# Kernel tuning notes

Hardware: AMD Instinct MI355X
Metric: run time of the kernel (lower is better)

## Reference

```python
import jax, jax.numpy as jnp
import numpy as np

N = 8192       # batch_size
D = 128        # embedding dim
C = 1000       # num classes
EPS = 1e-8     # torch CosineSimilarity eps


def setup_inputs() -> dict:
    key = jax.random.key(0)
    k1, k2, k3, k4 = jax.random.split(key, 4)
    inst_embed = jax.random.normal(k1, (N, D), dtype=jnp.float32)
    proxy = jax.random.normal(k2, (N, D), dtype=jnp.float32)
    # binary mask marking same-class (non-negative) pairs, stored as float
    negative_mask = (jax.random.uniform(k3, (N, C)) < 0.5).astype(jnp.float32)
    labels = jax.random.randint(k4, (N,), 0, C)
    temperature = jnp.float32(0.07)
    margin = jnp.float32(0.0)
    return {
        'inst_embed': inst_embed,
        'proxy': proxy,
        'negative_mask': negative_mask,
        'labels': labels,
        'temperature': temperature,
        'margin': margin,
    }


def _remove_diag(M):
    # M: [h, h] -> [h, h-1], dropping the diagonal, row-major order (as torch bool-mask view)
    h = M.shape[0]
    j = jnp.arange(h - 1)[None, :]
    i = jnp.arange(h)[:, None]
    cols = j + (j >= i)  # skip column i in row i
    return jnp.take_along_axis(M, cols, axis=1)


def _l2_normalize(x):
    return x / jnp.maximum(jnp.linalg.norm(x, axis=-1, keepdims=True), EPS)


def reference(inst_embed, proxy, negative_mask, labels, temperature, margin):
    negative_mask = negative_mask.T                       # [C, N]
    xn = _l2_normalize(inst_embed)                        # [N, D]
    sim = xn @ xn.T                                       # [N, N] cosine similarity matrix
    instance_zone = jnp.exp((_remove_diag(sim) - margin) / temperature)  # [N, N-1]
    pn = _l2_normalize(proxy)
    inst2proxy_positive = jnp.exp((jnp.sum(xn * pn, axis=-1) - margin) / temperature)  # [N]
    # pos_collected_numerator == True branch
    mask_4_remove_negatives = _remove_diag(negative_mask[labels])        # [N, N-1]
    inst2inst_positives = instance_zone * mask_4_remove_negatives
    numerator = inst2proxy_positive + inst2inst_positives.sum(axis=1)
    denominator = inst2proxy_positive + instance_zone.sum(axis=1)
    criterion = -jnp.log(temperature * (numerator / denominator)).mean()
    return criterion
```

## Files before the change

kernel.cpp:

```cpp
#include <hip/hip_runtime.h>
#include <hip/hip_bf16.h>

typedef unsigned short u16;
typedef unsigned int   u32;
typedef unsigned long long u64;
typedef __attribute__((ext_vector_type(8))) short short8;
typedef __attribute__((ext_vector_type(4))) float float4v;

#define N 8192
#define D 128
#define C 1000
#define TILE 128
#define LDT 136
#define NW64 (N / 64)
#define JQ 4
#define JW (JQ * 2)

__global__ void norm_kernel(const float* __restrict__ x, const float* __restrict__ pr,
                            u16* __restrict__ xnb, float* __restrict__ p_out,
                            float* __restrict__ den, float* __restrict__ num,
                            const float* __restrict__ tp, const float* __restrict__ mp) {
    const int wave = threadIdx.x >> 6;
    const int lane = threadIdx.x & 63;
    const int row  = blockIdx.x * 4 + wave;

    const float2* xr  = (const float2*)(x  + (size_t)row * D);
    const float2* prr = (const float2*)(pr + (size_t)row * D);
    float2 xv = xr[lane];
    float2 pv = prr[lane];

    float sx  = xv.x * xv.x + xv.y * xv.y;
    float sp  = pv.x * pv.x + pv.y * pv.y;
    float sxp = xv.x * pv.x + xv.y * pv.y;
    #pragma unroll
    for (int off = 32; off; off >>= 1) {
        sx  += __shfl_xor(sx,  off);
        sp  += __shfl_xor(sp,  off);
        sxp += __shfl_xor(sxp, off);
    }
    float nx = fmaxf(sqrtf(sx), 1e-8f);
    float np = fmaxf(sqrtf(sp), 1e-8f);
    float inv = 1.0f / nx;

    __hip_bfloat16 b0 = __float2bfloat16(xv.x * inv);
    __hip_bfloat16 b1 = __float2bfloat16(xv.y * inv);
    ((__hip_bfloat162*)xnb)[(size_t)row * 64 + lane] = __halves2bfloat162(b0, b1);

    if (lane == 0) {
        float T = tp[0], M = mp[0];
        p_out[row] = __expf((sxp / (nx * np) - M) / T);
        den[row] = 0.0f;
        num[row] = 0.0f;
    }
}

__global__ void pack_kernel(const float* __restrict__ nm, u64* __restrict__ packed) {
    __shared__ u32 Ls[64 * 65];
    const int lane = threadIdx.x & 63;
    const int wv   = threadIdx.x >> 6;
    const int jt   = blockIdx.x;
    const int lt   = blockIdx.y;
    const int j0   = jt * 64;
    const int l    = lt * 64 + lane;
    const bool lv  = l < C;

    #pragma unroll
    for (int rr = 0; rr < 16; rr++) {
        const int r = wv * 16 + rr;
        float v = lv ? nm[(size_t)(j0 + r) * C + l] : 0.0f;
        Ls[r * 65 + lane] = (v > 0.5f) ? 1u : 0u;
    }
    __syncthreads();
    #pragma unroll
    for (int cc = 0; cc < 16; cc++) {
        const int c = wv * 16 + cc;
        u64 m = __ballot(Ls[lane * 65 + c] != 0u);
        if (lane == 0 && (lt * 64 + c) < C)
            packed[(size_t)(lt * 64 + c) * NW64 + jt] = m;
    }
}

template <bool DIAG>
__device__ __forceinline__ void epilogue(const float4v acc[4][4], const u64* __restrict__ Ms,
                                         float dacc[4][4], float nacc[4][4],
                                         int wr, int wc, int kq, int m0,
                                         int ibase, int jbase, int q,
                                         float kA, float kB) {
    #pragma unroll
    for (int tm = 0; tm < 4; tm++) {
        #pragma unroll
        for (int r = 0; r < 4; r++) {
            const int lrow = wr * 64 + tm * 16 + kq * 4 + r;
            const u64 ws = Ms[lrow * JW + q * 2 + wc] >> m0;
            const u32 wlo = (u32)ws, whi = (u32)(ws >> 32);
            const int gi = ibase + lrow;
            #pragma unroll
            for (int tn = 0; tn < 4; tn++) {
                float e = __expf(fmaf(acc[tm][tn][r], kA, kB));
                if (DIAG) {
                    const int gj = jbase + wc * 64 + tn * 16 + m0;
                    if (gi == gj) e = 0.0f;
                }
                dacc[tm][r] += e;
                const u32 bit = ((tn < 2) ? (wlo >> (tn * 16)) : (whi >> ((tn - 2) * 16))) & 1u;
                nacc[tm][r] = fmaf((float)bit, e, nacc[tm][r]);
            }
        }
    }
}

__global__ __launch_bounds__(256, 2)
void cc_main(const u16* __restrict__ xnb, const int* __restrict__ labels,
             const u64* __restrict__ packed,
             float* __restrict__ den, float* __restrict__ num,
             const float* __restrict__ tp, const float* __restrict__ mp) {
    __shared__ u16 As[TILE * LDT];
    __shared__ u64 Ms[TILE * JW];

    const int tid  = threadIdx.x;
    const int lane = tid & 63;
    const int wv   = tid >> 6;
    const int wr   = wv >> 1;
    const int wc   = wv & 1;
    const int m0   = lane & 15;
    const int kq   = lane >> 4;
    const int ibase  = blockIdx.x * TILE;
    const int jsplit = blockIdx.y;

    const float T = tp[0];
    const float M = mp[0];
    const float kA = 1.0f / T;
    const float kB = -M / T;

    {
        const int r = tid >> 1, h = tid & 1;
        const uint4* src = (const uint4*)(xnb + (size_t)(ibase + r) * D + h * 64);
        uint4* dst = (uint4*)(As + r * LDT + h * 64);
        #pragma unroll
        for (int qq = 0; qq < 8; qq++) dst[qq] = src[qq];
    }
    #pragma unroll
    for (int t = 0; t < 4; t++) {
        const int idx = t * 256 + tid;
        const int row = idx >> 3, h = idx & 7;
        const int lab = labels[ibase + row];
        Ms[idx] = packed[(size_t)lab * NW64 + jsplit * JW + h];
    }
    __syncthreads();

    float dacc[4][4] = {};
    float nacc[4][4] = {};

    const u16* Abase = As + (wr * 64 + m0) * LDT + kq * 8;

    for (int q = 0; q < JQ; q++) {
        const int jt = jsplit * JQ + q;
        const int jbase = jt * TILE;

        const u16* Bp = xnb + (size_t)(jbase + wc * 64 + m0) * D + kq * 8;

        float4v acc[4][4];
        #pragma unroll
        for (int a = 0; a < 4; a++)
            #pragma unroll
            for (int b = 0; b < 4; b++)
                acc[a][b] = (float4v){0.f, 0.f, 0.f, 0.f};

        #pragma unroll
        for (int kk = 0; kk < 4; kk++) {
            short8 b_f[4];
            #pragma unroll
            for (int tn = 0; tn < 4; tn++)
                b_f[tn] = *(const short8*)(Bp + tn * (16 * D) + kk * 32);
            short8 a_f[4];
            #pragma unroll
            for (int tm = 0; tm < 4; tm++)
                a_f[tm] = *(const short8*)(Abase + tm * (16 * LDT) + kk * 32);
            #pragma unroll
            for (int tm = 0; tm < 4; tm++)
                #pragma unroll
                for (int tn = 0; tn < 4; tn++)
                    acc[tm][tn] = __builtin_amdgcn_mfma_f32_16x16x32_bf16(
                        a_f[tm], b_f[tn], acc[tm][tn], 0, 0, 0);
        }

        if (jt == blockIdx.x)
            epilogue<true >(acc, Ms, dacc, nacc, wr, wc, kq, m0, ibase, jbase, q, kA, kB);
        else
            epilogue<false>(acc, Ms, dacc, nacc, wr, wc, kq, m0, ibase, jbase, q, kA, kB);
    }

    #pragma unroll
    for (int tm = 0; tm < 4; tm++) {
        #pragma unroll
        for (int r = 0; r < 4; r++) {
            float d = dacc[tm][r], n = nacc[tm][r];
            #pragma unroll
            for (int off = 1; off < 16; off <<= 1) {
                d += __shfl_xor(d, off);
                n += __shfl_xor(n, off);
            }
            if (m0 == 0) {
                const int gi = ibase + wr * 64 + tm * 16 + kq * 4 + r;
                atomicAdd(&den[gi], d);
                atomicAdd(&num[gi], n);
            }
        }
    }
}

__global__ void loss_kernel(const float* __restrict__ p, const float* __restrict__ den,
                            const float* __restrict__ num, float* __restrict__ out,
                            const float* __restrict__ tp) {
    __shared__ float red[16];
    const float T = tp[0];
    float s = 0.0f;
    #pragma unroll
    for (int t = 0; t < N / 1024; t++) {
        const int i = t * 1024 + threadIdx.x;
        float pi = p[i];
        s += -__logf(T * (pi + num[i]) / (pi + den[i]));
    }
    #pragma unroll
    for (int off = 32; off; off >>= 1) s += __shfl_xor(s, off);
    const int lane = threadIdx.x & 63, wv = threadIdx.x >> 6;
    if (lane == 0) red[wv] = s;
    __syncthreads();
    if (wv == 0) {
        float t = (lane < 16) ? red[lane] : 0.0f;
        #pragma unroll
        for (int off = 8; off; off >>= 1) t += __shfl_xor(t, off);
        if (lane == 0) out[0] = t / (float)N;
    }
}

extern "C" void kernel_launch(void* const* d_in, const int* in_sizes, int n_in,
                              void* d_out, int out_size, void* d_ws, size_t ws_size,
                              hipStream_t stream) {
    (void)in_sizes; (void)n_in; (void)out_size; (void)ws_size;
    const float* inst   = (const float*)d_in[0];
    const float* proxy  = (const float*)d_in[1];
    const float* nm     = (const float*)d_in[2];
    const int*   labels = (const int*)d_in[3];
    const float* temp   = (const float*)d_in[4];
    const float* marg   = (const float*)d_in[5];
    float* out = (float*)d_out;

    char* ws = (char*)d_ws;
    u16*   xnb    = (u16*)ws;
    float* p_arr  = (float*)(ws + 2097152);
    u64*   packed = (u64*)(ws + 2129920);
    float* den    = (float*)(ws + 3153920);
    float* num    = (float*)(ws + 3186688);

    pack_kernel<<<dim3(N / 64, 16), 256, 0, stream>>>(nm, packed);
    norm_kernel<<<N / 4, 256, 0, stream>>>(inst, proxy, xnb, p_arr, den, num, temp, marg);
    cc_main<<<dim3(N / TILE, 16), 256, 0, stream>>>(xnb, labels, packed, den, num, temp, marg);
    loss_kernel<<<1, 1024, 0, stream>>>(p_arr, den, num, out, temp);
}
```

Measured before the change: 154.9 us.

## Drop LDS staging and give each wave an independent 32x64 tile

The main similarity kernel no longer stages the A tile and the label-mask words in shared memory. Each wave now owns 32 rows and sweeps 8 column chunks of 64, loading A and B fragments and the packed mask words straight from global memory. The smaller per-wave tile cuts register use, which allows 4 blocks per CU instead of 2 and removes the initial __syncthreads. In exchange, operand reuse drops: every wave reloads its own A rows and B tiles through cache, so the MFMA-to-load ratio falls and global/L2 traffic rises.

```diff
diff --git a/kernel.cpp b/kernel.cpp
--- a/kernel.cpp
+++ b/kernel.cpp
@@ -10,11 +10,8 @@
 #define N 8192
 #define D 128
 #define C 1000
-#define TILE 128
-#define LDT 136
 #define NW64 (N / 64)
-#define JQ 4
-#define JW (JQ * 2)
+#define JQ 8
 
 __global__ void norm_kernel(const float* __restrict__ x, const float* __restrict__ pr,
                             u16* __restrict__ xnb, float* __restrict__ p_out,
@@ -81,24 +78,24 @@
 }
 
 template <bool DIAG>
-__device__ __forceinline__ void epilogue(const float4v acc[4][4], const u64* __restrict__ Ms,
-                                         float dacc[4][4], float nacc[4][4],
-                                         int wr, int wc, int kq, int m0,
-                                         int ibase, int jbase, int q,
+__device__ __forceinline__ void epilogue(const float4v acc[2][4], const u64* __restrict__ packed,
+                                         const u32 offs[2][4],
+                                         float dacc[2][4], float nacc[2][4],
+                                         int kq, int m0, int rb, int jb, int q,
                                          float kA, float kB) {
     #pragma unroll
-    for (int tm = 0; tm < 4; tm++) {
+    for (int tm = 0; tm < 2; tm++) {
         #pragma unroll
         for (int r = 0; r < 4; r++) {
-            const int lrow = wr * 64 + tm * 16 + kq * 4 + r;
-            const u64 ws = Ms[lrow * JW + q * 2 + wc] >> m0;
+            const u64 w = packed[offs[tm][r] + q];
+            const u64 ws = w >> m0;
             const u32 wlo = (u32)ws, whi = (u32)(ws >> 32);
-            const int gi = ibase + lrow;
+            const int gi = rb + tm * 16 + kq * 4 + r;
             #pragma unroll
             for (int tn = 0; tn < 4; tn++) {
                 float e = __expf(fmaf(acc[tm][tn][r], kA, kB));
                 if (DIAG) {
-                    const int gj = jbase + wc * 64 + tn * 16 + m0;
+                    const int gj = jb + tn * 16 + m0;
                     if (gi == gj) e = 0.0f;
                 }
                 dacc[tm][r] += e;
@@ -109,59 +106,43 @@
     }
 }
 
-__global__ __launch_bounds__(256, 2)
+__global__ __launch_bounds__(256, 4)
 void cc_main(const u16* __restrict__ xnb, const int* __restrict__ labels,
              const u64* __restrict__ packed,
              float* __restrict__ den, float* __restrict__ num,
              const float* __restrict__ tp, const float* __restrict__ mp) {
-    __shared__ u16 As[TILE * LDT];
-    __shared__ u64 Ms[TILE * JW];
-
     const int tid  = threadIdx.x;
     const int lane = tid & 63;
     const int wv   = tid >> 6;
-    const int wr   = wv >> 1;
-    const int wc   = wv & 1;
     const int m0   = lane & 15;
     const int kq   = lane >> 4;
-    const int ibase  = blockIdx.x * TILE;
-    const int jsplit = blockIdx.y;
+    const int rb   = blockIdx.x * 128 + wv * 32;
+    const int jw0  = blockIdx.y * JQ;
 
     const float T = tp[0];
     const float M = mp[0];
     const float kA = 1.0f / T;
     const float kB = -M / T;
 
-    {
-        const int r = tid >> 1, h = tid & 1;
-        const uint4* src = (const uint4*)(xnb + (size_t)(ibase + r) * D + h * 64);
-        uint4* dst = (uint4*)(As + r * LDT + h * 64);
-        #pragma unroll
-        for (int qq = 0; qq < 8; qq++) dst[qq] = src[qq];
-    }
-    #pragma unroll
-    for (int t = 0; t < 4; t++) {
-        const int idx = t * 256 + tid;
-        const int row = idx >> 3, h = idx & 7;
-        const int lab = labels[ibase + row];
-        Ms[idx] = packed[(size_t)lab * NW64 + jsplit * JW + h];
-    }
-    __syncthreads();
-
-    float dacc[4][4] = {};
-    float nacc[4][4] = {};
-
-    const u16* Abase = As + (wr * 64 + m0) * LDT + kq * 8;
+    u32 offs[2][4];
+    #pragma unroll
+    for (int tm = 0; tm < 2; tm++)
+        #pragma unroll
+        for (int r = 0; r < 4; r++)
+            offs[tm][r] = (u32)labels[rb + tm * 16 + kq * 4 + r] * NW64 + jw0;
+
+    float dacc[2][4] = {};
+    float nacc[2][4] = {};
+
+    const u16* Ap = xnb + (size_t)(rb + m0) * D + kq * 8;
 
     for (int q = 0; q < JQ; q++) {
-        const int jt = jsplit * JQ + q;
-        const int jbase = jt * TILE;
-
-        const u16* Bp = xnb + (size_t)(jbase + wc * 64 + m0) * D + kq * 8;
-
-        float4v acc[4][4];
-        #pragma unroll
-        for (int a = 0; a < 4; a++)
+        const int jb = (jw0 + q) * 64;
+        const u16* Bp = xnb + (size_t)(jb + m0) * D + kq * 8;
+
+        float4v acc[2][4];
+        #pragma unroll
+        for (int a = 0; a < 2; a++)
             #pragma unroll
             for (int b = 0; b < 4; b++)
                 acc[a][b] = (float4v){0.f, 0.f, 0.f, 0.f};
@@ -172,26 +153,26 @@
             #pragma unroll
             for (int tn = 0; tn < 4; tn++)
                 b_f[tn] = *(const short8*)(Bp + tn * (16 * D) + kk * 32);
-            short8 a_f[4];
-            #pragma unroll
-            for (int tm = 0; tm < 4; tm++)
-                a_f[tm] = *(const short8*)(Abase + tm * (16 * LDT) + kk * 32);
-            #pragma unroll
-            for (int tm = 0; tm < 4; tm++)
+            short8 a_f[2];
+            #pragma unroll
+            for (int tm = 0; tm < 2; tm++)
+                a_f[tm] = *(const short8*)(Ap + tm * (16 * D) + kk * 32);
+            #pragma unroll
+            for (int tm = 0; tm < 2; tm++)
                 #pragma unroll
                 for (int tn = 0; tn < 4; tn++)
                     acc[tm][tn] = __builtin_amdgcn_mfma_f32_16x16x32_bf16(
                         a_f[tm], b_f[tn], acc[tm][tn], 0, 0, 0);
         }
 
-        if (jt == blockIdx.x)
-            epilogue<true >(acc, Ms, dacc, nacc, wr, wc, kq, m0, ibase, jbase, q, kA, kB);
+        if ((rb >> 6) == (jw0 + q))
+            epilogue<true >(acc, packed, offs, dacc, nacc, kq, m0, rb, jb, q, kA, kB);
         else
-            epilogue<false>(acc, Ms, dacc, nacc, wr, wc, kq, m0, ibase, jbase, q, kA, kB);
-    }
-
-    #pragma unroll
-    for (int tm = 0; tm < 4; tm++) {
+            epilogue<false>(acc, packed, offs, dacc, nacc, kq, m0, rb, jb, q, kA, kB);
+    }
+
+    #pragma unroll
+    for (int tm = 0; tm < 2; tm++) {
         #pragma unroll
         for (int r = 0; r < 4; r++) {
             float d = dacc[tm][r], n = nacc[tm][r];
@@ -201,7 +182,7 @@
                 n += __shfl_xor(n, off);
             }
             if (m0 == 0) {
-                const int gi = ibase + wr * 64 + tm * 16 + kq * 4 + r;
+                const int gi = rb + tm * 16 + kq * 4 + r;
                 atomicAdd(&den[gi], d);
                 atomicAdd(&num[gi], n);
             }
@@ -255,6 +236,6 @@
 
     pack_kernel<<<dim3(N / 64, 16), 256, 0, stream>>>(nm, packed);
     norm_kernel<<<N / 4, 256, 0, stream>>>(inst, proxy, xnb, p_arr, den, num, temp, marg);
-    cc_main<<<dim3(N / TILE, 16), 256, 0, stream>>>(xnb, labels, packed, den, num, temp, marg);
+    cc_main<<<dim3(N / 128, 16), 256, 0, stream>>>(xnb, labels, packed, den, num, temp, marg);
     loss_kernel<<<1, 1024, 0, stream>>>(p_arr, den, num, out, temp);
 }
```

New measurement: 196.7 us. 1.27x slower.

## Prefetch B fragments one k-step ahead, double j-tiles per block, use exp2

Applied to the files above, without the earlier changes.

B operand fragments are now software-pipelined: the loads for the next k-slice (or the first slice of the next j-tile) are issued before the current MFMAs, so global load latency overlaps compute. Each block now covers 8 j-tiles instead of 4, with the grid y-dimension halved and the label mask staging widened to match, which halves the per-block A-tile and mask setup and the atomics. The exponential is rewritten as a native exp2 with log2(e) folded into the scale constants. The cost is higher register pressure from the double-buffered fragments and fewer blocks to fill the GPU.

```diff
diff --git a/kernel.cpp b/kernel.cpp
--- a/kernel.cpp
+++ b/kernel.cpp
@@ -13,8 +13,9 @@
 #define TILE 128
 #define LDT 136
 #define NW64 (N / 64)
-#define JQ 4
+#define JQ 8
 #define JW (JQ * 2)
+#define LOG2E 1.44269504088896340736f
 
 __global__ void norm_kernel(const float* __restrict__ x, const float* __restrict__ pr,
                             u16* __restrict__ xnb, float* __restrict__ p_out,
@@ -85,7 +86,7 @@
                                          float dacc[4][4], float nacc[4][4],
                                          int wr, int wc, int kq, int m0,
                                          int ibase, int jbase, int q,
-                                         float kA, float kB) {
+                                         float kA2, float kB2) {
     #pragma unroll
     for (int tm = 0; tm < 4; tm++) {
         #pragma unroll
@@ -96,7 +97,7 @@
             const int gi = ibase + lrow;
             #pragma unroll
             for (int tn = 0; tn < 4; tn++) {
-                float e = __expf(fmaf(acc[tm][tn][r], kA, kB));
+                float e = __builtin_amdgcn_exp2f(fmaf(acc[tm][tn][r], kA2, kB2));
                 if (DIAG) {
                     const int gj = jbase + wc * 64 + tn * 16 + m0;
                     if (gi == gj) e = 0.0f;
@@ -126,11 +127,12 @@
     const int kq   = lane >> 4;
     const int ibase  = blockIdx.x * TILE;
     const int jsplit = blockIdx.y;
+    const int jt0    = jsplit * JQ;
 
     const float T = tp[0];
     const float M = mp[0];
-    const float kA = 1.0f / T;
-    const float kB = -M / T;
+    const float kA2 = LOG2E / T;
+    const float kB2 = -M * LOG2E / T;
 
     {
         const int r = tid >> 1, h = tid & 1;
@@ -140,11 +142,11 @@
         for (int qq = 0; qq < 8; qq++) dst[qq] = src[qq];
     }
     #pragma unroll
-    for (int t = 0; t < 4; t++) {
+    for (int t = 0; t < 8; t++) {
         const int idx = t * 256 + tid;
-        const int row = idx >> 3, h = idx & 7;
+        const int row = idx >> 4, h = idx & 15;
         const int lab = labels[ibase + row];
-        Ms[idx] = packed[(size_t)lab * NW64 + jsplit * JW + h];
+        Ms[idx] = packed[(size_t)lab * NW64 + jt0 * 2 + h];
     }
     __syncthreads();
 
@@ -152,12 +154,19 @@
     float nacc[4][4] = {};
 
     const u16* Abase = As + (wr * 64 + m0) * LDT + kq * 8;
+    const u16* Blane = xnb + (size_t)(wc * 64 + m0) * D + kq * 8;
+
+    short8 bc[4], bn[4];
+    {
+        const u16* Bp = Blane + (size_t)(jt0 * TILE) * D;
+        #pragma unroll
+        for (int tn = 0; tn < 4; tn++) bc[tn] = *(const short8*)(Bp + tn * (16 * D));
+    }
 
     for (int q = 0; q < JQ; q++) {
-        const int jt = jsplit * JQ + q;
+        const int jt = jt0 + q;
         const int jbase = jt * TILE;
-
-        const u16* Bp = xnb + (size_t)(jbase + wc * 64 + m0) * D + kq * 8;
+        const u16* Bq = Blane + (size_t)jbase * D;
 
         float4v acc[4][4];
         #pragma unroll
@@ -168,10 +177,16 @@
 
         #pragma unroll
         for (int kk = 0; kk < 4; kk++) {
-            short8 b_f[4];
-            #pragma unroll
-            for (int tn = 0; tn < 4; tn++)
-                b_f[tn] = *(const short8*)(Bp + tn * (16 * D) + kk * 32);
+            if (kk < 3) {
+                #pragma unroll
+                for (int tn = 0; tn < 4; tn++)
+                    bn[tn] = *(const short8*)(Bq + tn * (16 * D) + (kk + 1) * 32);
+            } else if (q < JQ - 1) {
+                const u16* Bnq = Bq + (size_t)TILE * D;
+                #pragma unroll
+                for (int tn = 0; tn < 4; tn++)
+                    bn[tn] = *(const short8*)(Bnq + tn * (16 * D));
+            }
             short8 a_f[4];
             #pragma unroll
             for (int tm = 0; tm < 4; tm++)
@@ -181,13 +196,15 @@
                 #pragma unroll
                 for (int tn = 0; tn < 4; tn++)
                     acc[tm][tn] = __builtin_amdgcn_mfma_f32_16x16x32_bf16(
-                        a_f[tm], b_f[tn], acc[tm][tn], 0, 0, 0);
+                        a_f[tm], bc[tn], acc[tm][tn], 0, 0, 0);
+            #pragma unroll
+            for (int tn = 0; tn < 4; tn++) bc[tn] = bn[tn];
         }
 
         if (jt == blockIdx.x)
-            epilogue<true >(acc, Ms, dacc, nacc, wr, wc, kq, m0, ibase, jbase, q, kA, kB);
+            epilogue<true >(acc, Ms, dacc, nacc, wr, wc, kq, m0, ibase, jbase, q, kA2, kB2);
         else
-            epilogue<false>(acc, Ms, dacc, nacc, wr, wc, kq, m0, ibase, jbase, q, kA, kB);
+            epilogue<false>(acc, Ms, dacc, nacc, wr, wc, kq, m0, ibase, jbase, q, kA2, kB2);
     }
 
     #pragma unroll
@@ -255,6 +272,6 @@
 
     pack_kernel<<<dim3(N / 64, 16), 256, 0, stream>>>(nm, packed);
     norm_kernel<<<N / 4, 256, 0, stream>>>(inst, proxy, xnb, p_arr, den, num, temp, marg);
-    cc_main<<<dim3(N / TILE, 16), 256, 0, stream>>>(xnb, labels, packed, den, num, temp, marg);
+    cc_main<<<dim3(N / TILE, 8), 256, 0, stream>>>(xnb, labels, packed, den, num, temp, marg);
     loss_kernel<<<1, 1024, 0, stream>>>(p_arr, den, num, out, temp);
 }
```

New measurement: 142.4 us. 8.1% less time.
